# Performance work log

Hardware: AMD Instinct MI355X
Metric: run time of the kernel (lower is better)

The kernel has to match this reference:

```python
import jax, jax.numpy as jnp
import numpy as np

DIM = 768
NUM_HEADS = 16
HEAD_DIM = DIM // NUM_HEADS  # 48


def setup_inputs() -> dict:
    key = jax.random.key(0)
    ks = jax.random.split(key, 9)
    s = 1.0 / np.sqrt(DIM)
    return {
        "x": jax.random.normal(ks[0], (4, 2048, DIM), dtype=jnp.float32),
        "Wq": jax.random.uniform(ks[1], (DIM, DIM), jnp.float32, -s, s),
        "bq": jax.random.uniform(ks[2], (DIM,), jnp.float32, -s, s),
        "Wk": jax.random.uniform(ks[3], (DIM, DIM), jnp.float32, -s, s),
        "bk": jax.random.uniform(ks[4], (DIM,), jnp.float32, -s, s),
        "Wv": jax.random.uniform(ks[5], (DIM, DIM), jnp.float32, -s, s),
        "bv": jax.random.uniform(ks[6], (DIM,), jnp.float32, -s, s),
        "Wo": jax.random.uniform(ks[7], (DIM, DIM), jnp.float32, -s, s),
        "bo": jax.random.uniform(ks[8], (DIM,), jnp.float32, -s, s),
    }


def reference(x, Wq, bq, Wk, bk, Wv, bv, Wo, bo):
    B, S, D = x.shape
    H, Dh = NUM_HEADS, HEAD_DIM
    # qkv projections -> [B, H, S, Dh]
    q = (x @ Wq.T + bq).reshape(B, S, H, Dh).transpose(0, 2, 1, 3)
    k = (x @ Wk.T + bk).reshape(B, S, H, Dh).transpose(0, 2, 1, 3)
    v = (x @ Wv.T + bv).reshape(B, S, H, Dh).transpose(0, 2, 1, 3)
    scale = 1.0 / np.sqrt(Dh).astype(np.float32)
    scores = jnp.einsum('bhqd,bhkd->bhqk', q, k) * scale  # [B,H,S,S]
    attn = jax.nn.softmax(scores, axis=-1)
    # dropout is identity in eval mode
    out = jnp.einsum('bhqk,bhkd->bhqd', attn, v)  # [B,H,S,Dh]
    out = out.transpose(0, 2, 1, 3).reshape(B, S, D)
    return out @ Wo.T + bo
```

## Files before the change

### kernel.cpp

```cpp
#include <hip/hip_runtime.h>
#include <cstdint>
#include <cstddef>


typedef short s8v __attribute__((ext_vector_type(8)));
typedef float f4v __attribute__((ext_vector_type(4)));

static constexpr int Bn = 4, Sn = 2048, Dn = 768, Hn = 16, DhN = 48, Dp = 64;
static constexpr int MS = Bn * Sn;

#define MFMA16(a, b, c) __builtin_amdgcn_mfma_f32_16x16x32_bf16((a), (b), (c), 0, 0, 0)

__device__ __forceinline__ int swz4(int r) { return (r + (r >> 2)) & 3; }

__device__ __forceinline__ ushort f2b(float f) {
  return (ushort)((__builtin_bit_cast(uint32_t, f) + 0x8000u) >> 16);
}
__device__ __forceinline__ uint32_t packbf(float a, float b) {
  uint32_t ua = __builtin_bit_cast(uint32_t, a) + 0x8000u;
  uint32_t ub = __builtin_bit_cast(uint32_t, b) + 0x8000u;
  return __builtin_amdgcn_perm(ub, ua, 0x07060302u);
}
__device__ __forceinline__ float fexp2(float x) {
  return __builtin_amdgcn_exp2f(x);
}
__device__ __forceinline__ void gload_lds16(const ushort* g, ushort* l) {
  __builtin_amdgcn_global_load_lds(
      (const __attribute__((address_space(1))) uint32_t*)g,
      (__attribute__((address_space(3))) uint32_t*)l, 16, 0, 0);
}

__global__ void cvt_all(const float* __restrict__ x,
                        const float* __restrict__ wq, const float* __restrict__ wk,
                        const float* __restrict__ wv, const float* __restrict__ wo,
                        ushort* __restrict__ xb, ushort* __restrict__ wqkv,
                        ushort* __restrict__ wob) {
  const int bid = blockIdx.x;
  const float* src;
  ushort* dst;
  int i;
  if (bid < 6144) {
    src = x; dst = xb; i = bid * 256 + threadIdx.x;
  } else {
    const int r = (bid - 6144) / 576;
    i = ((bid - 6144) % 576) * 256 + threadIdx.x;
    src = (r == 0) ? wq : (r == 1) ? wk : (r == 2) ? wv : wo;
    dst = (r < 3) ? (wqkv + (size_t)r * Dn * Dn) : wob;
  }
  float4 f = ((const float4*)src)[i];
  ushort4 o = { f2b(f.x), f2b(f.y), f2b(f.z), f2b(f.w) };
  ((ushort4*)dst)[i] = o;
}

__global__ __launch_bounds__(256) void gemm_qkv(
    const ushort* __restrict__ A, const ushort* __restrict__ W,
    const float* __restrict__ bq, const float* __restrict__ bk, const float* __restrict__ bv,
    ushort* __restrict__ outq, ushort* __restrict__ outk, ushort* __restrict__ outv,
    float qscale) {
  __shared__ __align__(16) ushort As[128][32];
  __shared__ __align__(16) ushort Bs[128][32];
  const int tid = threadIdx.x, lane = tid & 63, wave = tid >> 6;
  const int l15 = lane & 15, g = lane >> 4;
  const int m0 = blockIdx.y * 128, n0 = blockIdx.x * 128;
  const int wqm = (wave >> 1) * 64;
  const int wqx = (wave & 1) * 64;
  f4v acc[4][4] = {};

  const int slot0 = wave * 128 + lane;
  const int slot1 = slot0 + 64;
  const int r0 = slot0 >> 2, u0 = ((slot0 & 3) ^ swz4(r0 & 15)) * 8;
  const int r1 = slot1 >> 2, u1 = ((slot1 & 3) ^ swz4(r1 & 15)) * 8;
  const ushort* ag0 = A + (size_t)(m0 + r0) * Dn + u0;
  const ushort* ag1 = A + (size_t)(m0 + r1) * Dn + u1;
  const ushort* bg0 = W + (size_t)(n0 + r0) * Dn + u0;
  const ushort* bg1 = W + (size_t)(n0 + r1) * Dn + u1;
  ushort* lA0 = &As[0][0] + slot0 * 8;
  ushort* lA1 = &As[0][0] + slot1 * 8;
  ushort* lB0 = &Bs[0][0] + slot0 * 8;
  ushort* lB1 = &Bs[0][0] + slot1 * 8;
  const int fcol = (g ^ swz4(l15)) * 8;

  for (int k0 = 0; k0 < Dn; k0 += 32) {
    __syncthreads();
    gload_lds16(ag0 + k0, lA0);
    gload_lds16(ag1 + k0, lA1);
    gload_lds16(bg0 + k0, lB0);
    gload_lds16(bg1 + k0, lB1);
    __syncthreads();
    s8v wf[4], xf[4];
#pragma unroll
    for (int i = 0; i < 4; ++i) wf[i] = *(const s8v*)&Bs[wqm + i * 16 + l15][fcol];
#pragma unroll
    for (int j = 0; j < 4; ++j) xf[j] = *(const s8v*)&As[wqx + j * 16 + l15][fcol];
#pragma unroll
    for (int i = 0; i < 4; ++i)
#pragma unroll
      for (int j = 0; j < 4; ++j) acc[i][j] = MFMA16(wf[i], xf[j], acc[i][j]);
  }

  const int region = blockIdx.x / 6;
  const int nbase = n0 - region * 768;
  const float* bias = (region == 0) ? bq : (region == 1) ? bk : bv;
#pragma unroll
  for (int i = 0; i < 4; ++i) {
    const int n = nbase + wqm + i * 16 + g * 4;
    const float4 b4 = *(const float4*)&bias[n];
    const int h = n / DhN, dh = n - h * DhN;
#pragma unroll
    for (int j = 0; j < 4; ++j) {
      const int s = m0 + wqx + j * 16 + l15;
      const int b = s >> 11, srow = s & 2047;
      const int bh = b * Hn + h;
      float v0 = acc[i][j][0] + b4.x, v1 = acc[i][j][1] + b4.y;
      float v2 = acc[i][j][2] + b4.z, v3 = acc[i][j][3] + b4.w;
      if (region == 0) { v0 *= qscale; v1 *= qscale; v2 *= qscale; v3 *= qscale; }
      if (region < 2) {
        ushort4 o = { f2b(v0), f2b(v1), f2b(v2), f2b(v3) };
        ushort* dst = region ? outk : outq;
        const size_t base = ((size_t)bh * Sn + srow) * Dp;
        *(ushort4*)&dst[base + dh] = o;
        if (region == 0 && dh < 4) {
          const uint4 z = {0, 0, 0, 0};
          *(uint4*)&dst[base + 48] = z;
          *(uint4*)&dst[base + 56] = z;
        }
      } else {
        outv[((size_t)bh * DhN + dh + 0) * Sn + srow] = f2b(v0);
        outv[((size_t)bh * DhN + dh + 1) * Sn + srow] = f2b(v1);
        outv[((size_t)bh * DhN + dh + 2) * Sn + srow] = f2b(v2);
        outv[((size_t)bh * DhN + dh + 3) * Sn + srow] = f2b(v3);
      }
    }
  }
}

__global__ __launch_bounds__(256) void gemm_out(
    const ushort* __restrict__ A, const ushort* __restrict__ W,
    const float* __restrict__ bias, float* __restrict__ out) {
  __shared__ __align__(16) ushort As[128][32];
  __shared__ __align__(16) ushort Bs[128][32];
  const int tid = threadIdx.x, lane = tid & 63, wave = tid >> 6;
  const int l15 = lane & 15, g = lane >> 4;
  const int m0 = blockIdx.y * 128, n0 = blockIdx.x * 128;
  const int wqm = (wave >> 1) * 64;
  const int wqx = (wave & 1) * 64;
  f4v acc[4][4] = {};

  const int slot0 = wave * 128 + lane;
  const int slot1 = slot0 + 64;
  const int r0 = slot0 >> 2, u0 = ((slot0 & 3) ^ swz4(r0 & 15)) * 8;
  const int r1 = slot1 >> 2, u1 = ((slot1 & 3) ^ swz4(r1 & 15)) * 8;
  const ushort* ag0 = A + (size_t)(m0 + r0) * Dn + u0;
  const ushort* ag1 = A + (size_t)(m0 + r1) * Dn + u1;
  const ushort* bg0 = W + (size_t)(n0 + r0) * Dn + u0;
  const ushort* bg1 = W + (size_t)(n0 + r1) * Dn + u1;
  ushort* lA0 = &As[0][0] + slot0 * 8;
  ushort* lA1 = &As[0][0] + slot1 * 8;
  ushort* lB0 = &Bs[0][0] + slot0 * 8;
  ushort* lB1 = &Bs[0][0] + slot1 * 8;
  const int fcol = (g ^ swz4(l15)) * 8;

  for (int k0 = 0; k0 < Dn; k0 += 32) {
    __syncthreads();
    gload_lds16(ag0 + k0, lA0);
    gload_lds16(ag1 + k0, lA1);
    gload_lds16(bg0 + k0, lB0);
    gload_lds16(bg1 + k0, lB1);
    __syncthreads();
    s8v wf[4], xf[4];
#pragma unroll
    for (int i = 0; i < 4; ++i) wf[i] = *(const s8v*)&Bs[wqm + i * 16 + l15][fcol];
#pragma unroll
    for (int j = 0; j < 4; ++j) xf[j] = *(const s8v*)&As[wqx + j * 16 + l15][fcol];
#pragma unroll
    for (int i = 0; i < 4; ++i)
#pragma unroll
      for (int j = 0; j < 4; ++j) acc[i][j] = MFMA16(wf[i], xf[j], acc[i][j]);
  }

#pragma unroll
  for (int i = 0; i < 4; ++i) {
    const int n = n0 + wqm + i * 16 + g * 4;
    const float4 b4 = *(const float4*)&bias[n];
#pragma unroll
    for (int j = 0; j < 4; ++j) {
      const int s = m0 + wqx + j * 16 + l15;
      float4 o4 = { acc[i][j][0] + b4.x, acc[i][j][1] + b4.y,
                    acc[i][j][2] + b4.z, acc[i][j][3] + b4.w };
      *(float4*)&out[(size_t)s * Dn + n] = o4;
    }
  }
}

__global__ __launch_bounds__(256) void attn_kernel(
    const ushort* __restrict__ qg, const ushort* __restrict__ kg,
    const ushort* __restrict__ vg, ushort* __restrict__ og) {
  __shared__ __align__(16) ushort Ks[2][64][32];
  __shared__ __align__(16) ushort Vs[2][64][32];
  __shared__ __align__(16) ushort Ps[4][32][40];
  const int tid = threadIdx.x;
  const int lane = tid & 63;
  const int wave = tid >> 6;
  const int l15 = lane & 15;
  const int g = lane >> 4;
  const int bh = blockIdx.y;
  const int q0 = blockIdx.x * 128;
  const ushort* qb = qg + (size_t)bh * Sn * Dp;
  const ushort* kb = kg + (size_t)bh * Sn * Dp;
  const ushort* vb = vg + (size_t)bh * DhN * Sn;

#pragma unroll
  for (int t = 0; t < 2; ++t) {
    const int idx = tid + t * 256;
    const int half = idx >> 8;
    const int rem = idx & 255;
    const int row = 48 + (rem >> 4);
    const int col = (rem & 15) * 2;
    *(uint32_t*)&Vs[half][row][col] = (row == 48) ? 0x3F803F80u : 0u;
  }

  s8v qa[2][2];
#pragma unroll
  for (int nt = 0; nt < 2; ++nt)
#pragma unroll
    for (int kc = 0; kc < 2; ++kc)
      qa[nt][kc] = *(const s8v*)(qb + (size_t)(q0 + wave * 32 + nt * 16 + l15) * Dp + kc * 32 + g * 8);

  const int lr = lane >> 2, lc = lane & 3;
  const int lcs = (lc ^ swz4(lr)) * 8;
  const ushort* gsrc[4];
  ushort* ldst[4];
  int gstep[4];
  const int nchunk = (wave < 2) ? 4 : 3;
#pragma unroll
  for (int t = 0; t < 4; ++t) {
    const int c = wave + 4 * t;
    if (c < 8) {
      const int half = c >> 2, rr = (c & 3) * 16;
      gsrc[t] = kb + (size_t)(rr + lr) * Dp + half * 32 + lcs;
      ldst[t] = &Ks[half][rr][0] + lane * 8;
      gstep[t] = 64 * Dp;
    } else if (c < 14) {
      const int cc = c - 8;
      const int half = cc >= 3 ? 1 : 0;
      const int rr = (cc - half * 3) * 16;
      gsrc[t] = vb + (size_t)(rr + lr) * Sn + half * 32 + lcs;
      ldst[t] = &Vs[half][rr][0] + lane * 8;
      gstep[t] = 64;
    } else {
      gsrc[t] = nullptr; ldst[t] = nullptr; gstep[t] = 0;
    }
  }

  const int fcol = (g ^ swz4(l15)) * 8;
  f4v acc[2][4] = {};

  for (int kt = 0; kt < Sn; kt += 64) {
    __syncthreads();
    for (int t = 0; t < nchunk; ++t) {
      gload_lds16(gsrc[t], ldst[t]);
      gsrc[t] += gstep[t];
    }
    __syncthreads();

#pragma unroll
    for (int half = 0; half < 2; ++half) {
#pragma unroll
      for (int lmt = 0; lmt < 2; ++lmt) {
        const int mt = half * 2 + lmt;
        s8v ka0 = *(const s8v*)&Ks[0][mt * 16 + l15][fcol];
        s8v ka1 = *(const s8v*)&Ks[1][mt * 16 + l15][fcol];
#pragma unroll
        for (int nt = 0; nt < 2; ++nt) {
          f4v z = {};
          z = MFMA16(ka0, qa[nt][0], z);
          f4v st = MFMA16(ka1, qa[nt][1], z);
          const float p0 = fexp2(st[0]), p1 = fexp2(st[1]);
          const float p2 = fexp2(st[2]), p3 = fexp2(st[3]);
          uint2 pw;
          pw.x = packbf(p0, p1);
          pw.y = packbf(p2, p3);
          *(uint2*)&Ps[wave][nt * 16 + l15][lmt * 16 + g * 4] = pw;
        }
      }
      s8v vf[4];
#pragma unroll
      for (int d = 0; d < 4; ++d) vf[d] = *(const s8v*)&Vs[half][d * 16 + l15][fcol];
#pragma unroll
      for (int nt = 0; nt < 2; ++nt) {
        s8v pa = *(const s8v*)&Ps[wave][nt * 16 + l15][g * 8];
#pragma unroll
        for (int d = 0; d < 4; ++d) acc[nt][d] = MFMA16(pa, vf[d], acc[nt][d]);
      }
    }
  }

  const int b = bh >> 4, h = bh & 15;
#pragma unroll
  for (int nt = 0; nt < 2; ++nt) {
#pragma unroll
    for (int r = 0; r < 4; ++r) {
      const float lq = __shfl(acc[nt][3][r], g * 16, 64);
      const float inv = 1.0f / lq;
      const int s = q0 + wave * 32 + nt * 16 + g * 4 + r;
      const size_t base = ((size_t)(b * Sn + s)) * Dn + h * DhN;
#pragma unroll
      for (int d = 0; d < 3; ++d)
        og[base + d * 16 + l15] = f2b(acc[nt][d][r] * inv);
    }
  }
}

extern "C" void kernel_launch(void* const* d_in, const int* in_sizes, int n_in,
                              void* d_out, int out_size, void* d_ws, size_t ws_size,
                              hipStream_t stream) {
  (void)in_sizes; (void)n_in; (void)out_size; (void)ws_size;
  const float* x  = (const float*)d_in[0];
  const float* Wq = (const float*)d_in[1];
  const float* bq = (const float*)d_in[2];
  const float* Wk = (const float*)d_in[3];
  const float* bk = (const float*)d_in[4];
  const float* Wv = (const float*)d_in[5];
  const float* bv = (const float*)d_in[6];
  const float* Wo = (const float*)d_in[7];
  const float* bo = (const float*)d_in[8];

  size_t off = 0;
  auto alloc = [&](size_t bytes) {
    void* p = (char*)d_ws + off;
    off += (bytes + 255) & ~(size_t)255;
    return p;
  };
  ushort* xb    = (ushort*)alloc((size_t)MS * Dn * 2);
  ushort* Wqkvb = (ushort*)alloc((size_t)3 * Dn * Dn * 2);
  ushort* Wob   = (ushort*)alloc((size_t)Dn * Dn * 2);
  ushort* qbuf  = (ushort*)alloc((size_t)Bn * Hn * Sn * Dp * 2);
  ushort* kbuf  = (ushort*)alloc((size_t)Bn * Hn * Sn * Dp * 2);
  ushort* vbuf  = (ushort*)alloc((size_t)Bn * Hn * DhN * Sn * 2);
  ushort* ao    = (ushort*)alloc((size_t)MS * Dn * 2);

  cvt_all<<<6144 + 4 * 576, 256, 0, stream>>>(x, Wq, Wk, Wv, Wo, xb, Wqkvb, Wob);

  const dim3 blk(256);
  const float qscale = 0.20823510929813633f;
  gemm_qkv<<<dim3(18, MS / 128), blk, 0, stream>>>(xb, Wqkvb, bq, bk, bv,
                                                   qbuf, kbuf, vbuf, qscale);

  attn_kernel<<<dim3(Sn / 128, Bn * Hn), blk, 0, stream>>>(qbuf, kbuf, vbuf, ao);

  gemm_out<<<dim3(6, MS / 128), blk, 0, stream>>>(ao, Wob, bo, (float*)d_out);
}
```

Baseline: 259.5 us.

## Switch attention to 32x32x16 MFMA with register-resident P and 48-wide QK

The attention kernel now uses 32x32x16 bf16 MFMAs. QK^T reduces over only the 48 real head dims (three k-chunks) instead of the zero-padded 64, and probabilities are moved into the PV A-operand through a cross-half wave shuffle instead of a round trip through LDS. K and V tiles get new XOR-swizzled LDS layouts, with a ones row in V still supplying the softmax denominator. The zero-fill of Q padding columns is dropped from the projection kernel because padding is no longer read. This cuts MFMA count and LDS traffic per tile but adds cross-lane shuffles and a more complex output layout.

```diff
diff --git a/kernel.cpp b/kernel.cpp
--- a/kernel.cpp
+++ b/kernel.cpp
@@ -5,11 +5,13 @@
 
 typedef short s8v __attribute__((ext_vector_type(8)));
 typedef float f4v __attribute__((ext_vector_type(4)));
+typedef float f16v __attribute__((ext_vector_type(16)));
 
 static constexpr int Bn = 4, Sn = 2048, Dn = 768, Hn = 16, DhN = 48, Dp = 64;
 static constexpr int MS = Bn * Sn;
 
 #define MFMA16(a, b, c) __builtin_amdgcn_mfma_f32_16x16x32_bf16((a), (b), (c), 0, 0, 0)
+#define MFMA32(a, b, c) __builtin_amdgcn_mfma_f32_32x32x16_bf16((a), (b), (c), 0, 0, 0)
 
 __device__ __forceinline__ int swz4(int r) { return (r + (r >> 2)) & 3; }
 
@@ -117,13 +119,7 @@
       if (region < 2) {
         ushort4 o = { f2b(v0), f2b(v1), f2b(v2), f2b(v3) };
         ushort* dst = region ? outk : outq;
-        const size_t base = ((size_t)bh * Sn + srow) * Dp;
-        *(ushort4*)&dst[base + dh] = o;
-        if (region == 0 && dh < 4) {
-          const uint4 z = {0, 0, 0, 0};
-          *(uint4*)&dst[base + 48] = z;
-          *(uint4*)&dst[base + 56] = z;
-        }
+        *(ushort4*)&dst[((size_t)bh * Sn + srow) * Dp + dh] = o;
       } else {
         outv[((size_t)bh * DhN + dh + 0) * Sn + srow] = f2b(v0);
         outv[((size_t)bh * DhN + dh + 1) * Sn + srow] = f2b(v1);
@@ -195,14 +191,14 @@
 __global__ __launch_bounds__(256) void attn_kernel(
     const ushort* __restrict__ qg, const ushort* __restrict__ kg,
     const ushort* __restrict__ vg, ushort* __restrict__ og) {
-  __shared__ __align__(16) ushort Ks[2][64][32];
-  __shared__ __align__(16) ushort Vs[2][64][32];
-  __shared__ __align__(16) ushort Ps[4][32][40];
+  __shared__ __align__(16) ushort Ka[64][32];
+  __shared__ __align__(16) ushort Kb[64][16];
+  __shared__ __align__(16) ushort Vs[64][64];
   const int tid = threadIdx.x;
   const int lane = tid & 63;
   const int wave = tid >> 6;
-  const int l15 = lane & 15;
-  const int g = lane >> 4;
+  const int l31 = lane & 31;
+  const int h = lane >> 5;
   const int bh = blockIdx.y;
   const int q0 = blockIdx.x * 128;
   const ushort* qb = qg + (size_t)bh * Sn * Dp;
@@ -212,102 +208,100 @@
 #pragma unroll
   for (int t = 0; t < 2; ++t) {
     const int idx = tid + t * 256;
-    const int half = idx >> 8;
-    const int rem = idx & 255;
-    const int row = 48 + (rem >> 4);
-    const int col = (rem & 15) * 2;
-    *(uint32_t*)&Vs[half][row][col] = (row == 48) ? 0x3F803F80u : 0u;
-  }
-
-  s8v qa[2][2];
-#pragma unroll
-  for (int nt = 0; nt < 2; ++nt)
-#pragma unroll
-    for (int kc = 0; kc < 2; ++kc)
-      qa[nt][kc] = *(const s8v*)(qb + (size_t)(q0 + wave * 32 + nt * 16 + l15) * Dp + kc * 32 + g * 8);
-
-  const int lr = lane >> 2, lc = lane & 3;
-  const int lcs = (lc ^ swz4(lr)) * 8;
-  const ushort* gsrc[4];
-  ushort* ldst[4];
-  int gstep[4];
-  const int nchunk = (wave < 2) ? 4 : 3;
-#pragma unroll
-  for (int t = 0; t < 4; ++t) {
+    const int row = 48 + (idx >> 5);
+    ((uint32_t*)&Vs[row][0])[idx & 31] = (row == 48) ? 0x3F803F80u : 0u;
+  }
+
+  s8v qf[3];
+#pragma unroll
+  for (int kc = 0; kc < 3; ++kc)
+    qf[kc] = *(const s8v*)(qb + (size_t)(q0 + wave * 32 + l31) * Dp + kc * 16 + h * 8);
+
+  const ushort* gsrc[3];
+  ushort* ldst[3];
+  int gstep[3];
+#pragma unroll
+  for (int t = 0; t < 3; ++t) {
     const int c = wave + 4 * t;
-    if (c < 8) {
-      const int half = c >> 2, rr = (c & 3) * 16;
-      gsrc[t] = kb + (size_t)(rr + lr) * Dp + half * 32 + lcs;
-      ldst[t] = &Ks[half][rr][0] + lane * 8;
+    if (c < 4) {
+      const int row = 16 * c + (lane >> 2), j = lane & 3;
+      gsrc[t] = kb + (size_t)row * Dp + (j ^ ((row >> 1) & 3)) * 8;
+      ldst[t] = &Ka[0][0] + 16 * c * 32 + lane * 8;
       gstep[t] = 64 * Dp;
-    } else if (c < 14) {
-      const int cc = c - 8;
-      const int half = cc >= 3 ? 1 : 0;
-      const int rr = (cc - half * 3) * 16;
-      gsrc[t] = vb + (size_t)(rr + lr) * Sn + half * 32 + lcs;
-      ldst[t] = &Vs[half][rr][0] + lane * 8;
+    } else if (c < 6) {
+      const int row = 32 * (c - 4) + (lane >> 1), j = lane & 1;
+      gsrc[t] = kb + (size_t)row * Dp + 32 + (j ^ ((row >> 2) & 1)) * 8;
+      ldst[t] = &Kb[0][0] + 32 * (c - 4) * 16 + lane * 8;
+      gstep[t] = 64 * Dp;
+    } else {
+      const int row = 8 * (c - 6) + (lane >> 3), j = lane & 7;
+      gsrc[t] = vb + (size_t)row * Sn + (j ^ (row & 7)) * 8;
+      ldst[t] = &Vs[0][0] + 8 * (c - 6) * 64 + lane * 8;
       gstep[t] = 64;
-    } else {
-      gsrc[t] = nullptr; ldst[t] = nullptr; gstep[t] = 0;
-    }
-  }
-
-  const int fcol = (g ^ swz4(l15)) * 8;
-  f4v acc[2][4] = {};
+    }
+  }
+
+  f16v o0 = {}, o1 = {};
 
   for (int kt = 0; kt < Sn; kt += 64) {
     __syncthreads();
-    for (int t = 0; t < nchunk; ++t) {
+#pragma unroll
+    for (int t = 0; t < 3; ++t) {
       gload_lds16(gsrc[t], ldst[t]);
       gsrc[t] += gstep[t];
     }
     __syncthreads();
 
 #pragma unroll
-    for (int half = 0; half < 2; ++half) {
-#pragma unroll
-      for (int lmt = 0; lmt < 2; ++lmt) {
-        const int mt = half * 2 + lmt;
-        s8v ka0 = *(const s8v*)&Ks[0][mt * 16 + l15][fcol];
-        s8v ka1 = *(const s8v*)&Ks[1][mt * 16 + l15][fcol];
-#pragma unroll
-        for (int nt = 0; nt < 2; ++nt) {
-          f4v z = {};
-          z = MFMA16(ka0, qa[nt][0], z);
-          f4v st = MFMA16(ka1, qa[nt][1], z);
-          const float p0 = fexp2(st[0]), p1 = fexp2(st[1]);
-          const float p2 = fexp2(st[2]), p3 = fexp2(st[3]);
-          uint2 pw;
-          pw.x = packbf(p0, p1);
-          pw.y = packbf(p2, p3);
-          *(uint2*)&Ps[wave][nt * 16 + l15][lmt * 16 + g * 4] = pw;
-        }
+    for (int mg = 0; mg < 2; ++mg) {
+      const int row = 32 * mg + l31;
+      const int s1 = (l31 >> 1) & 3, s2 = (l31 >> 2) & 1;
+      s8v a0 = *(const s8v*)&Ka[row][((0 | h) ^ s1) * 8];
+      s8v a1 = *(const s8v*)&Ka[row][((2 | h) ^ s1) * 8];
+      s8v a2 = *(const s8v*)&Kb[row][((h) ^ s2) * 8];
+      f16v sc = {};
+      sc = MFMA32(a0, qf[0], sc);
+      sc = MFMA32(a1, qf[1], sc);
+      sc = MFMA32(a2, qf[2], sc);
+      float p[16];
+#pragma unroll
+      for (int r = 0; r < 16; ++r) p[r] = fexp2(sc[r]);
+
+#pragma unroll
+      for (int c2 = 0; c2 < 2; ++c2) {
+        const int rb = 8 * c2;
+        const uint32_t lo0 = packbf(p[rb + 0], p[rb + 1]);
+        const uint32_t lo1 = packbf(p[rb + 2], p[rb + 3]);
+        const uint32_t hi0 = packbf(p[rb + 4], p[rb + 5]);
+        const uint32_t hi1 = packbf(p[rb + 6], p[rb + 7]);
+        const uint32_t t0 = __shfl_xor(h ? lo0 : hi0, 32, 64);
+        const uint32_t t1 = __shfl_xor(h ? lo1 : hi1, 32, 64);
+        uint4 af;
+        af.x = h ? t0 : lo0;
+        af.y = h ? t1 : lo1;
+        af.z = h ? hi0 : t0;
+        af.w = h ? hi1 : t1;
+        const s8v pa = __builtin_bit_cast(s8v, af);
+        const int kcv = 2 * mg + c2;
+        const int vc = ((2 * kcv + h) ^ (l31 & 7)) * 8;
+        const s8v v0 = *(const s8v*)&Vs[l31][vc];
+        const s8v v1 = *(const s8v*)&Vs[32 + l31][vc];
+        o0 = MFMA32(pa, v0, o0);
+        o1 = MFMA32(pa, v1, o1);
       }
-      s8v vf[4];
-#pragma unroll
-      for (int d = 0; d < 4; ++d) vf[d] = *(const s8v*)&Vs[half][d * 16 + l15][fcol];
-#pragma unroll
-      for (int nt = 0; nt < 2; ++nt) {
-        s8v pa = *(const s8v*)&Ps[wave][nt * 16 + l15][g * 8];
-#pragma unroll
-        for (int d = 0; d < 4; ++d) acc[nt][d] = MFMA16(pa, vf[d], acc[nt][d]);
-      }
-    }
-  }
-
-  const int b = bh >> 4, h = bh & 15;
-#pragma unroll
-  for (int nt = 0; nt < 2; ++nt) {
-#pragma unroll
-    for (int r = 0; r < 4; ++r) {
-      const float lq = __shfl(acc[nt][3][r], g * 16, 64);
-      const float inv = 1.0f / lq;
-      const int s = q0 + wave * 32 + nt * 16 + g * 4 + r;
-      const size_t base = ((size_t)(b * Sn + s)) * Dn + h * DhN;
-#pragma unroll
-      for (int d = 0; d < 3; ++d)
-        og[base + d * 16 + l15] = f2b(acc[nt][d][r] * inv);
-    }
+    }
+  }
+
+  const int b = bh >> 4, hh = bh & 15;
+#pragma unroll
+  for (int r = 0; r < 16; ++r) {
+    const int q = (r & 3) + 8 * (r >> 2) + 4 * h;
+    const float lsum = __shfl(o1[r], 16 + (lane & 32), 64);
+    const float inv = 1.0f / lsum;
+    const int s = q0 + wave * 32 + q;
+    const size_t base = ((size_t)(b * Sn + s)) * Dn + hh * DhN;
+    og[base + l31] = f2b(o0[r] * inv);
+    if (l31 < 16) og[base + 32 + l31] = f2b(o1[r] * inv);
   }
 }
 
```

Result: faster. 252.4 us (-2.7%).
